# Kernel tuning notes

Hardware: AMD Instinct MI355X
Metric: run time of the kernel (lower is better)

Reference implementation:

```python
import jax, jax.numpy as jnp
import numpy as np
from jax import lax

B, T, E, H = 256, 512, 256, 256

def setup_inputs() -> dict:
    key = jax.random.key(0)
    k1, k2, k3, k4, k5 = jax.random.split(key, 5)
    s_in = 1.0 / np.sqrt(E)
    s_h = 1.0 / np.sqrt(H)
    return {
        "x": jax.random.normal(k1, (B, T, E), dtype=jnp.float32),
        "Wx_w": jax.random.normal(k2, (H, E), dtype=jnp.float32) * s_in,
        "Wx_b": jax.random.normal(k3, (H,), dtype=jnp.float32) * s_in,
        "Wh_w": jax.random.normal(k4, (H, H), dtype=jnp.float32) * s_h,
        "Wh_b": jax.random.normal(k5, (H,), dtype=jnp.float32) * s_h,
    }

def reference(x, Wx_w, Wx_b, Wh_w, Wh_b):
    # Precompute input gates for all timesteps: g = sigmoid(Wx(x))  [B,T,H]
    gates = jax.nn.sigmoid(jnp.einsum("bte,he->bth", x, Wx_w) + Wx_b)
    h0 = jnp.zeros((x.shape[0], Wh_w.shape[0]), dtype=x.dtype)

    def step(h, g_t):  # g_t: [B,H]
        h_new = h * g_t + (1.0 - g_t) * jnp.tanh(h @ Wh_w.T + Wh_b)
        return h_new, h_new

    _, outs = lax.scan(step, h0, jnp.swapaxes(gates, 0, 1))  # [T,B,H]
    return jnp.swapaxes(outs, 0, 1)  # [B,T,H]
```

## Files before the change

kernel.cpp:

```cpp
#include <hip/hip_runtime.h>

#define Tsz 512
#define Hsz 256

typedef __attribute__((ext_vector_type(8))) short short8;
typedef __attribute__((ext_vector_type(4))) short short4v;
typedef __attribute__((ext_vector_type(4))) float f32x4;

static __device__ __forceinline__ unsigned short f2bf(float f) {
    union { float f; unsigned int i; } v; v.f = f;
    unsigned int r = v.i + 0x7fffu + ((v.i >> 16) & 1u);
    return (unsigned short)(r >> 16);
}
static __device__ __forceinline__ short8 ld8f(const float* p) {
    const float4* q = (const float4*)p;
    float4 a = q[0], b = q[1];
    short8 v;
    v[0] = (short)f2bf(a.x); v[1] = (short)f2bf(a.y); v[2] = (short)f2bf(a.z); v[3] = (short)f2bf(a.w);
    v[4] = (short)f2bf(b.x); v[5] = (short)f2bf(b.y); v[6] = (short)f2bf(b.z); v[7] = (short)f2bf(b.w);
    return v;
}
static __device__ __forceinline__ float sigm(float z) {
    return __builtin_amdgcn_rcpf(1.f + __expf(-z));
}

__global__ __launch_bounds__(256) void cvt_wx(const float* __restrict__ Wxw,
                                              unsigned short* __restrict__ wxbf)
{
    int i = (blockIdx.x * 256 + threadIdx.x) * 4;
    float4 v = *(const float4*)(Wxw + i);
    short4v s4;
    s4[0] = (short)f2bf(v.x); s4[1] = (short)f2bf(v.y);
    s4[2] = (short)f2bf(v.z); s4[3] = (short)f2bf(v.w);
    *(short4v*)(wxbf + i) = s4;
}

__global__ __launch_bounds__(512, 2) void mgu_fused(
    const float* __restrict__ x,   const unsigned short* __restrict__ wxbf,
    const float* __restrict__ Wxb, const float* __restrict__ Whw,
    const float* __restrict__ Whb, float* __restrict__ out)
{
    __shared__ __align__(16) unsigned short xs[2][16 * 256];
    __shared__ __align__(16) float          gs[2][16 * 256];
    __shared__ __align__(16) unsigned short hbuf[2][256];

    const int tid  = threadIdx.x;
    const int b    = blockIdx.x;
    const int l    = tid & 63;
    const int w    = tid >> 6;
    const int lo16 = l & 15;
    const int hi   = l >> 4;

    short8 wfh[2][8];
    float  bh[2], bx[2];
#pragma unroll
    for (int nt = 0; nt < 2; ++nt) {
        int n = w * 32 + nt * 16 + lo16;
        bh[nt] = Whb[n];
        bx[nt] = Wxb[n];
#pragma unroll
        for (int ks = 0; ks < 8; ++ks)
            wfh[nt][ks] = ld8f(Whw + (size_t)n * 256 + ks * 32 + hi * 8);
    }

    const unsigned short* gwb = wxbf + (size_t)(w * 32 + lo16) * 256 + hi * 8;

    const float* xrow = x   + (size_t)b * Tsz * Hsz;
    float*       orow = out + (size_t)b * Tsz * Hsz;

#pragma unroll
    for (int i = 0; i < 4; ++i) {
        int idx = tid + i * 512;
        int m   = idx >> 6;
        int j   = idx & 63;
        float4 v = *(const float4*)(xrow + (size_t)m * 256 + j * 4);
        short4v s4;
        s4[0] = (short)f2bf(v.x); s4[1] = (short)f2bf(v.y);
        s4[2] = (short)f2bf(v.z); s4[3] = (short)f2bf(v.w);
        int r   = m & 15;
        int byt = r * 512 + (((j >> 1) ^ (r & 7)) << 4) + (j & 1) * 8;
        *(short4v*)((char*)xs[m >> 4] + byt) = s4;
    }
    if (tid < 256) hbuf[0][tid] = 0;
    __syncthreads();

    {
        f32x4 ag0 = {0.f, 0.f, 0.f, 0.f}, ag1 = {0.f, 0.f, 0.f, 0.f};
#pragma unroll
        for (int ks = 0; ks < 8; ++ks) {
            short8 afg = *(const short8*)((const char*)xs[0]
                           + lo16 * 512 + (((ks * 4 + hi) ^ (lo16 & 7)) << 4));
            short8 b0 = *(const short8*)(gwb + ks * 32);
            short8 b1 = *(const short8*)(gwb + 16 * 256 + ks * 32);
            ag0 = __builtin_amdgcn_mfma_f32_16x16x32_bf16(afg, b0, ag0, 0, 0, 0);
            ag1 = __builtin_amdgcn_mfma_f32_16x16x32_bf16(afg, b1, ag1, 0, 0, 0);
        }
#pragma unroll
        for (int r = 0; r < 4; ++r) {
            gs[0][(hi * 4 + r) * 256 + w * 32 + lo16]      = sigm(ag0[r] + bx[0]);
            gs[0][(hi * 4 + r) * 256 + w * 32 + 16 + lo16] = sigm(ag1[r] + bx[1]);
        }
    }

    float  hreg = 0.f;
    float4 xcarry;
    if (tid < 64) xcarry = *(const float4*)(xrow + (size_t)32 * 256 + tid * 4);

    f32x4 accg[2];
    { f32x4 z = {0.f, 0.f, 0.f, 0.f}; accg[0] = z; accg[1] = z; }

    int p = 0;
    for (int c = 0; c < 32; ++c) {
        const char*  xs_rd = (const char*)xs[(c & 1) ^ 1];
        char*        xs_wr = (char*)xs[c & 1];
        const float* gs_rd = gs[c & 1];
        float*       gs_wr = gs[(c & 1) ^ 1];
        short8 afg;
#pragma unroll
        for (int s = 0; s < 16; ++s) {
            const int t = c * 16 + s;
            __syncthreads();

            short8 gbf = *(const short8*)(gwb + (s & 1) * (16 * 256) + (s >> 1) * 32);

            const int n_ep = w * 32 + (hi & 1) * 16 + lo16;
            float g = gs_rd[s * 256 + n_ep];

            if ((s & 1) == 0)
                afg = *(const short8*)(xs_rd
                        + lo16 * 512 + ((((s >> 1) * 4 + hi) ^ (lo16 & 7)) << 4));

            f32x4 a0lo = {bh[0], 0.f, 0.f, 0.f}, a0hi = {0.f, 0.f, 0.f, 0.f};
            f32x4 a1lo = {bh[1], 0.f, 0.f, 0.f}, a1hi = {0.f, 0.f, 0.f, 0.f};
            {
                short8 afh[4];
#pragma unroll
                for (int ks = 0; ks < 4; ++ks)
                    afh[ks] = *(const short8*)(const void*)(&hbuf[p][ks * 32 + hi * 8]);
#pragma unroll
                for (int ks = 0; ks < 4; ++ks) {
                    a0lo = __builtin_amdgcn_mfma_f32_16x16x32_bf16(afh[ks], wfh[0][ks], a0lo, 0, 0, 0);
                    a1lo = __builtin_amdgcn_mfma_f32_16x16x32_bf16(afh[ks], wfh[1][ks], a1lo, 0, 0, 0);
                }
            }
            {
                short8 afh[4];
#pragma unroll
                for (int ks = 0; ks < 4; ++ks)
                    afh[ks] = *(const short8*)(const void*)(&hbuf[p][(ks + 4) * 32 + hi * 8]);
#pragma unroll
                for (int ks = 0; ks < 4; ++ks) {
                    a0hi = __builtin_amdgcn_mfma_f32_16x16x32_bf16(afh[ks], wfh[0][ks + 4], a0hi, 0, 0, 0);
                    a1hi = __builtin_amdgcn_mfma_f32_16x16x32_bf16(afh[ks], wfh[1][ks + 4], a1hi, 0, 0, 0);
                }
            }

            accg[s & 1] = __builtin_amdgcn_mfma_f32_16x16x32_bf16(afg, gbf, accg[s & 1], 0, 0, 0);

            if (tid < 64) {
                short4v s4;
                s4[0] = (short)f2bf(xcarry.x); s4[1] = (short)f2bf(xcarry.y);
                s4[2] = (short)f2bf(xcarry.z); s4[3] = (short)f2bf(xcarry.w);
                int byt = s * 512 + (((tid >> 1) ^ (s & 7)) << 4) + (tid & 1) * 8;
                *(short4v*)(xs_wr + byt) = s4;
                int nr = t + 33; if (nr > Tsz - 1) nr = Tsz - 1;
                xcarry = *(const float4*)(xrow + (size_t)nr * 256 + tid * 4);
            }

            float zz = (hi == 0) ? (a0lo[0] + a0hi[0]) : (a1lo[0] + a1hi[0]);
            zz = fminf(fmaxf(zz, -15.f), 15.f);
            float ex = __expf(2.f * zz);
            float th = (ex - 1.f) * __builtin_amdgcn_rcpf(ex + 1.f);
            if (hi < 2) {
                float hn = g * hreg + (1.f - g) * th;
                hreg = hn;
                hbuf[p ^ 1][n_ep] = f2bf(hn);
                orow[(size_t)t * 256 + n_ep] = hn;
            }

            if (s == 15) {
#pragma unroll
                for (int r = 0; r < 4; ++r) {
                    gs_wr[(hi * 4 + r) * 256 + w * 32 + lo16]      = sigm(accg[0][r] + bx[0]);
                    gs_wr[(hi * 4 + r) * 256 + w * 32 + 16 + lo16] = sigm(accg[1][r] + bx[1]);
                }
                f32x4 z = {0.f, 0.f, 0.f, 0.f}; accg[0] = z; accg[1] = z;
            }
            p ^= 1;
        }
    }
}

extern "C" void kernel_launch(void* const* d_in, const int* in_sizes, int n_in,
                              void* d_out, int out_size, void* d_ws, size_t ws_size,
                              hipStream_t stream) {
    const float* x   = (const float*)d_in[0];
    const float* Wxw = (const float*)d_in[1];
    const float* Wxb = (const float*)d_in[2];
    const float* Whw = (const float*)d_in[3];
    const float* Whb = (const float*)d_in[4];
    unsigned short* wxbf = (unsigned short*)d_ws;

    cvt_wx<<<dim3(64), dim3(256), 0, stream>>>(Wxw, wxbf);
    mgu_fused<<<dim3(256), dim3(512), 0, stream>>>(x, wxbf, Wxb, Whw, Whb, (float*)d_out);
}
```

Baseline: 277.7 us.

## Spread x prefetch across all threads, store gates as bf16, pad x tile

Only the first 64 threads used to load one x row per step. Now the next chunk of x is staged by all 512 threads in two bulk loads per 16-step chunk, with the load and the conversion spaced four steps apart to hide latency. The gate buffer in shared memory is stored as bf16 instead of fp32, and each step prefetches the next step's gate into a register. The XOR swizzle on the x tile is replaced by row padding. This trades some gate precision and adds a register for a smaller shared-memory footprint and less per-step work in the serial recurrence.

```diff
diff --git a/kernel.cpp b/kernel.cpp
--- a/kernel.cpp
+++ b/kernel.cpp
@@ -11,6 +11,9 @@
     union { float f; unsigned int i; } v; v.f = f;
     unsigned int r = v.i + 0x7fffu + ((v.i >> 16) & 1u);
     return (unsigned short)(r >> 16);
+}
+static __device__ __forceinline__ float bf2f(unsigned short u) {
+    union { unsigned int i; float f; } v; v.i = ((unsigned int)u) << 16; return v.f;
 }
 static __device__ __forceinline__ short8 ld8f(const float* p) {
     const float4* q = (const float4*)p;
@@ -35,13 +38,14 @@
     *(short4v*)(wxbf + i) = s4;
 }
 
+#define XP 264
 __global__ __launch_bounds__(512, 2) void mgu_fused(
     const float* __restrict__ x,   const unsigned short* __restrict__ wxbf,
     const float* __restrict__ Wxb, const float* __restrict__ Whw,
     const float* __restrict__ Whb, float* __restrict__ out)
 {
-    __shared__ __align__(16) unsigned short xs[2][16 * 256];
-    __shared__ __align__(16) float          gs[2][16 * 256];
+    __shared__ __align__(16) unsigned short xs[2][16 * XP];
+    __shared__ __align__(16) unsigned short gsb[2][16 * 256];
     __shared__ __align__(16) unsigned short hbuf[2][256];
 
     const int tid  = threadIdx.x;
@@ -50,6 +54,7 @@
     const int w    = tid >> 6;
     const int lo16 = l & 15;
     const int hi   = l >> 4;
+    const int n_ep = w * 32 + (hi & 1) * 16 + lo16;
 
     short8 wfh[2][8];
     float  bh[2], bx[2];
@@ -67,6 +72,9 @@
 
     const float* xrow = x   + (size_t)b * Tsz * Hsz;
     float*       orow = out + (size_t)b * Tsz * Hsz;
+
+    const int srow = tid >> 6;
+    const int sj   = tid & 63;
 
 #pragma unroll
     for (int i = 0; i < 4; ++i) {
@@ -77,9 +85,7 @@
         short4v s4;
         s4[0] = (short)f2bf(v.x); s4[1] = (short)f2bf(v.y);
         s4[2] = (short)f2bf(v.z); s4[3] = (short)f2bf(v.w);
-        int r   = m & 15;
-        int byt = r * 512 + (((j >> 1) ^ (r & 7)) << 4) + (j & 1) * 8;
-        *(short4v*)((char*)xs[m >> 4] + byt) = s4;
+        *(short4v*)(&xs[m >> 4][(m & 15) * XP + j * 4]) = s4;
     }
     if (tid < 256) hbuf[0][tid] = 0;
     __syncthreads();
@@ -88,8 +94,7 @@
         f32x4 ag0 = {0.f, 0.f, 0.f, 0.f}, ag1 = {0.f, 0.f, 0.f, 0.f};
 #pragma unroll
         for (int ks = 0; ks < 8; ++ks) {
-            short8 afg = *(const short8*)((const char*)xs[0]
-                           + lo16 * 512 + (((ks * 4 + hi) ^ (lo16 & 7)) << 4));
+            short8 afg = *(const short8*)(&xs[0][lo16 * XP + ks * 32 + hi * 8]);
             short8 b0 = *(const short8*)(gwb + ks * 32);
             short8 b1 = *(const short8*)(gwb + 16 * 256 + ks * 32);
             ag0 = __builtin_amdgcn_mfma_f32_16x16x32_bf16(afg, b0, ag0, 0, 0, 0);
@@ -97,38 +102,55 @@
         }
 #pragma unroll
         for (int r = 0; r < 4; ++r) {
-            gs[0][(hi * 4 + r) * 256 + w * 32 + lo16]      = sigm(ag0[r] + bx[0]);
-            gs[0][(hi * 4 + r) * 256 + w * 32 + 16 + lo16] = sigm(ag1[r] + bx[1]);
+            gsb[0][(hi * 4 + r) * 256 + w * 32 + lo16]      = f2bf(sigm(ag0[r] + bx[0]));
+            gsb[0][(hi * 4 + r) * 256 + w * 32 + 16 + lo16] = f2bf(sigm(ag1[r] + bx[1]));
         }
     }
 
     float  hreg = 0.f;
-    float4 xcarry;
-    if (tid < 64) xcarry = *(const float4*)(xrow + (size_t)32 * 256 + tid * 4);
-
+    float  g_carry = 0.f;
+    float4 stg;
     f32x4 accg[2];
     { f32x4 z = {0.f, 0.f, 0.f, 0.f}; accg[0] = z; accg[1] = z; }
-
-    int p = 0;
+    short8 afg;
+
     for (int c = 0; c < 32; ++c) {
-        const char*  xs_rd = (const char*)xs[(c & 1) ^ 1];
-        char*        xs_wr = (char*)xs[c & 1];
-        const float* gs_rd = gs[c & 1];
-        float*       gs_wr = gs[(c & 1) ^ 1];
-        short8 afg;
+        unsigned short*       xs_rd = xs[(c & 1) ^ 1];
+        unsigned short*       xs_wr = xs[c & 1];
+        const unsigned short* gs_rd = gsb[c & 1];
+        unsigned short*       gs_wr = gsb[(c & 1) ^ 1];
 #pragma unroll
         for (int s = 0; s < 16; ++s) {
-            const int t = c * 16 + s;
+            const int pp = s & 1;
+            const int t  = c * 16 + s;
             __syncthreads();
 
-            short8 gbf = *(const short8*)(gwb + (s & 1) * (16 * 256) + (s >> 1) * 32);
-
-            const int n_ep = w * 32 + (hi & 1) * 16 + lo16;
-            float g = gs_rd[s * 256 + n_ep];
+            float g = (s == 0) ? bf2f(gs_rd[n_ep]) : g_carry;
+            if (s < 15) g_carry = bf2f(gs_rd[(s + 1) * 256 + n_ep]);
+
+            short8 gbf = *(const short8*)(gwb + pp * (16 * 256) + (s >> 1) * 32);
 
             if ((s & 1) == 0)
-                afg = *(const short8*)(xs_rd
-                        + lo16 * 512 + ((((s >> 1) * 4 + hi) ^ (lo16 & 7)) << 4));
+                afg = *(const short8*)(&xs_rd[lo16 * XP + (s >> 1) * 32 + hi * 8]);
+
+            if (c < 30) {
+                if (s == 0)
+                    stg = *(const float4*)(xrow + (size_t)((c + 2) * 16 + srow) * 256 + sj * 4);
+                if (s == 4) {
+                    short4v s4;
+                    s4[0] = (short)f2bf(stg.x); s4[1] = (short)f2bf(stg.y);
+                    s4[2] = (short)f2bf(stg.z); s4[3] = (short)f2bf(stg.w);
+                    *(short4v*)(&xs_wr[srow * XP + sj * 4]) = s4;
+                }
+                if (s == 8)
+                    stg = *(const float4*)(xrow + (size_t)((c + 2) * 16 + 8 + srow) * 256 + sj * 4);
+                if (s == 12) {
+                    short4v s4;
+                    s4[0] = (short)f2bf(stg.x); s4[1] = (short)f2bf(stg.y);
+                    s4[2] = (short)f2bf(stg.z); s4[3] = (short)f2bf(stg.w);
+                    *(short4v*)(&xs_wr[(8 + srow) * XP + sj * 4]) = s4;
+                }
+            }
 
             f32x4 a0lo = {bh[0], 0.f, 0.f, 0.f}, a0hi = {0.f, 0.f, 0.f, 0.f};
             f32x4 a1lo = {bh[1], 0.f, 0.f, 0.f}, a1hi = {0.f, 0.f, 0.f, 0.f};
@@ -136,7 +158,7 @@
                 short8 afh[4];
 #pragma unroll
                 for (int ks = 0; ks < 4; ++ks)
-                    afh[ks] = *(const short8*)(const void*)(&hbuf[p][ks * 32 + hi * 8]);
+                    afh[ks] = *(const short8*)(const void*)(&hbuf[pp][ks * 32 + hi * 8]);
 #pragma unroll
                 for (int ks = 0; ks < 4; ++ks) {
                     a0lo = __builtin_amdgcn_mfma_f32_16x16x32_bf16(afh[ks], wfh[0][ks], a0lo, 0, 0, 0);
@@ -147,7 +169,7 @@
                 short8 afh[4];
 #pragma unroll
                 for (int ks = 0; ks < 4; ++ks)
-                    afh[ks] = *(const short8*)(const void*)(&hbuf[p][(ks + 4) * 32 + hi * 8]);
+                    afh[ks] = *(const short8*)(const void*)(&hbuf[pp][(ks + 4) * 32 + hi * 8]);
 #pragma unroll
                 for (int ks = 0; ks < 4; ++ks) {
                     a0hi = __builtin_amdgcn_mfma_f32_16x16x32_bf16(afh[ks], wfh[0][ks + 4], a0hi, 0, 0, 0);
@@ -155,17 +177,7 @@
                 }
             }
 
-            accg[s & 1] = __builtin_amdgcn_mfma_f32_16x16x32_bf16(afg, gbf, accg[s & 1], 0, 0, 0);
-
-            if (tid < 64) {
-                short4v s4;
-                s4[0] = (short)f2bf(xcarry.x); s4[1] = (short)f2bf(xcarry.y);
-                s4[2] = (short)f2bf(xcarry.z); s4[3] = (short)f2bf(xcarry.w);
-                int byt = s * 512 + (((tid >> 1) ^ (s & 7)) << 4) + (tid & 1) * 8;
-                *(short4v*)(xs_wr + byt) = s4;
-                int nr = t + 33; if (nr > Tsz - 1) nr = Tsz - 1;
-                xcarry = *(const float4*)(xrow + (size_t)nr * 256 + tid * 4);
-            }
+            accg[pp] = __builtin_amdgcn_mfma_f32_16x16x32_bf16(afg, gbf, accg[pp], 0, 0, 0);
 
             float zz = (hi == 0) ? (a0lo[0] + a0hi[0]) : (a1lo[0] + a1hi[0]);
             zz = fminf(fmaxf(zz, -15.f), 15.f);
@@ -174,19 +186,18 @@
             if (hi < 2) {
                 float hn = g * hreg + (1.f - g) * th;
                 hreg = hn;
-                hbuf[p ^ 1][n_ep] = f2bf(hn);
+                hbuf[pp ^ 1][n_ep] = f2bf(hn);
                 orow[(size_t)t * 256 + n_ep] = hn;
             }
 
             if (s == 15) {
 #pragma unroll
                 for (int r = 0; r < 4; ++r) {
-                    gs_wr[(hi * 4 + r) * 256 + w * 32 + lo16]      = sigm(accg[0][r] + bx[0]);
-                    gs_wr[(hi * 4 + r) * 256 + w * 32 + 16 + lo16] = sigm(accg[1][r] + bx[1]);
+                    gs_wr[(hi * 4 + r) * 256 + w * 32 + lo16]      = f2bf(sigm(accg[0][r] + bx[0]));
+                    gs_wr[(hi * 4 + r) * 256 + w * 32 + 16 + lo16] = f2bf(sigm(accg[1][r] + bx[1]));
                 }
                 f32x4 z = {0.f, 0.f, 0.f, 0.f}; accg[0] = z; accg[1] = z;
             }
-            p ^= 1;
         }
     }
 }
```

After: 237.8 us. 14.3% less time.
